# Performance work log

Hardware: AMD Instinct MI355X
Metric: run time of the kernel (lower is better)

## Reference

```python
import jax, jax.numpy as jnp
import numpy as np

BOS, EOS, MAX_STEPS = 1, 2, 50
VOCAB, EMBD, HID, CTX, SEQ = 50257, 512, 1024, 1024, 50


def setup_inputs() -> dict:
    key = jax.random.key(0)
    ks = jax.random.split(key, 13)
    s = 0.05
    return {
        "seq_enc_states": jax.random.normal(ks[0], (SEQ, 1, CTX), jnp.float32),
        "seq_enc_hidden": jax.random.normal(ks[1], (1, CTX), jnp.float32),
        "E": jax.random.normal(ks[2], (VOCAB, EMBD), jnp.float32) * s,
        "W_init": jax.random.normal(ks[3], (HID, CTX), jnp.float32) * s,
        "b_init": jax.random.normal(ks[4], (HID,), jnp.float32) * s,
        "Wa": jax.random.normal(ks[5], (CTX, HID), jnp.float32) * s,
        "ba": jax.random.normal(ks[6], (CTX,), jnp.float32) * s,
        "W_ih": jax.random.normal(ks[7], (3 * HID, EMBD + CTX), jnp.float32) * s,
        "W_hh": jax.random.normal(ks[8], (3 * HID, HID), jnp.float32) * s,
        "b_ih": jax.random.normal(ks[9], (3 * HID,), jnp.float32) * s,
        "b_hh": jax.random.normal(ks[10], (3 * HID,), jnp.float32) * s,
        "Wv": jax.random.normal(ks[11], (VOCAB, HID), jnp.float32) * s,
        "bv": jax.random.normal(ks[12], (VOCAB,), jnp.float32) * s,
    }


def _gru_cell(x, h, W_ih, W_hh, b_ih, b_hh):
    # torch.nn.GRUCell math
    gi = x @ W_ih.T + b_ih  # (1, 3H)
    gh = h @ W_hh.T + b_hh  # (1, 3H)
    i_r, i_z, i_n = jnp.split(gi, 3, axis=-1)
    h_r, h_z, h_n = jnp.split(gh, 3, axis=-1)
    r = jax.nn.sigmoid(i_r + h_r)
    z = jax.nn.sigmoid(i_z + h_z)
    n = jnp.tanh(i_n + r * h_n)
    return (1.0 - z) * n + z * h


def reference(seq_enc_states, seq_enc_hidden, E, W_init, b_init, Wa, ba,
              W_ih, W_hh, b_ih, b_hh, Wv, bv):
    enc = seq_enc_states[:, 0, :]                       # (S, CTX)
    h0 = seq_enc_hidden.reshape(1, -1) @ W_init.T + b_init  # (1, H)
    emb0 = E[BOS][None, :]                              # (1, EMBD)

    def step(carry, _):
        h, emb, done = carry
        # dot-product attention over the 50 encoder positions
        ph = h @ Wa.T + ba                              # (1, CTX)
        attn = jax.nn.softmax(ph @ enc.T, axis=-1)      # (1, S)
        ctx = attn @ enc                                # (1, CTX)
        x = jnp.concatenate([emb, ctx], axis=-1)        # (1, EMBD+CTX)
        h_new = _gru_cell(x, h, W_ih, W_hh, b_ih, b_hh)
        logp = jax.nn.log_softmax(h_new @ Wv.T + bv, axis=-1)  # (1, V)
        idx = jnp.argmax(logp[0])
        valid = jnp.logical_not(done)
        is_eos = idx == EOS
        emit_idx = jnp.where(valid & jnp.logical_not(is_eos), idx, -1).astype(jnp.int32)
        logp_out = jnp.where(valid, logp[0], 0.0)
        new_emb = jnp.where((valid & jnp.logical_not(is_eos))[..., None], E[idx][None, :], emb)
        new_h = jnp.where(valid, h_new, h)
        new_done = done | is_eos
        return (new_h, new_emb, new_done), (emit_idx, logp_out, valid)

    init = (h0, emb0, jnp.array(False))
    _, (indices, logps, valid) = jax.lax.scan(step, init, None, length=MAX_STEPS)
    # indices: (50,) int32, -1 where past eos / eos itself (not appended in original)
    return indices, logps, valid
```

## Files before the change

kernel.cpp:

```cpp
#include <hip/hip_runtime.h>
#include <hip/hip_fp16.h>
#include <cmath>

#define VOCABSZ 50257
#define EMBD 512
#define HIDD 1024
#define CTXD 1024
#define SEQL 50
#define NSTEPS 50
#define BOS_ID 1
#define EOS_ID 2

#define NTHR 256
#define NB_GI 768
#define NB_WR 64
#define NB_LOG 832
#define NW_LOG (NB_LOG * 4)
#define NB_GHN 192
#define KL_ATTN NB_LOG
#define KL_GH0 (NB_LOG + 1)
#define KL_WR0 (NB_LOG + 1 + NB_GHN)
#define KL_GRID (KL_WR0 + NB_WR)
#define PRE_GRID (NB_GI + 1)
#define PRE_GRID_FIN (NB_GI + 1 + NB_WR)

#define LPAD 50304

#define OFF_M      0
#define OFF_T      51200
#define OFF_H      51264
#define OFF_CTX    53312
#define OFF_GI     54336
#define OFF_GH     57408
#define OFF_L      63552
#define OFF_STATS  164160
#define OFF_STATE  170816
#define OFF_WVH    171072

__device__ __forceinline__ float wred_sum(float v) {
#pragma unroll
  for (int o = 32; o > 0; o >>= 1) v += __shfl_xor(v, o, 64);
  return v;
}

__device__ __forceinline__ float dot4(float4 a, float4 b) {
  return a.x * b.x + a.y * b.y + a.z * b.z + a.w * b.w;
}

__device__ __forceinline__ float wdot1024(const float* __restrict__ row, int lane,
                                          float4 b0, float4 b1, float4 b2, float4 b3) {
  const float4* r = (const float4*)row;
  float acc = dot4(r[lane], b0) + dot4(r[lane + 64], b1) +
              dot4(r[lane + 128], b2) + dot4(r[lane + 192], b3);
  return wred_sum(acc);
}

__device__ __forceinline__ bool beats(float v, int i, float v0, int i0) {
  return v > v0 || (v == v0 && i < i0);
}

__device__ __forceinline__ void top2_merge(float& v1, int& i1, float& v2, int& i2,
                                           float w1, int j1, float w2, int j2) {
  if (beats(w1, j1, v1, i1)) {
    float nv2; int ni2;
    if (beats(v1, i1, w2, j2)) { nv2 = v1; ni2 = i1; } else { nv2 = w2; ni2 = j2; }
    v1 = w1; i1 = j1; v2 = nv2; i2 = ni2;
  } else if (beats(w1, j1, v2, i2)) {
    v2 = w1; i2 = j1;
  }
}

__device__ __forceinline__ float acc8(uint4 a, const float* b) {
  const __half2* h = reinterpret_cast<const __half2*>(&a);
  float2 f0 = __half22float2(h[0]);
  float2 f1 = __half22float2(h[1]);
  float2 f2 = __half22float2(h[2]);
  float2 f3 = __half22float2(h[3]);
  return f0.x * b[0] + f0.y * b[1] + f1.x * b[2] + f1.y * b[3] +
         f2.x * b[4] + f2.y * b[5] + f3.x * b[6] + f3.y * b[7];
}

__global__ void __launch_bounds__(NTHR)
k_cvt(const float4* __restrict__ src, uint2* __restrict__ dst, int n4) {
  int i = blockIdx.x * NTHR + threadIdx.x;
  const int stride = gridDim.x * NTHR;
  for (; i < n4; i += stride) {
    float4 v = src[i];
    __half2 a = __floats2half2_rn(v.x, v.y);
    __half2 b = __floats2half2_rn(v.z, v.w);
    uint2 u;
    u.x = *reinterpret_cast<unsigned*>(&a);
    u.y = *reinterpret_cast<unsigned*>(&b);
    dst[i] = u;
  }
}

__global__ void __launch_bounds__(1024)
k0_matM(float* __restrict__ ws, const float* __restrict__ enc,
        const float* __restrict__ Wa) {
  const int kc = blockIdx.x;
  const int jg = blockIdx.y;
  const int tid = threadIdx.x;
  const int w = tid >> 6, lane = tid & 63;
  const int jw = w & 3, q = w >> 2;
  const int j = jg * 4 + jw;
  const int k = kc * 64 + lane;
  __shared__ float s_red[16][64];
  float acc0 = 0.f, acc1 = 0.f, acc2 = 0.f, acc3 = 0.f;
  if (j < SEQL) {
    const float4* e4 = (const float4*)(enc + (size_t)j * CTXD);
    const float* Wc = Wa + k;
    for (int c4 = q * 64; c4 < q * 64 + 64; ++c4) {
      float4 e = e4[c4];
      const float* wp = Wc + (size_t)(c4 * 4) * HIDD;
      acc0 += e.x * wp[0];
      acc1 += e.y * wp[HIDD];
      acc2 += e.z * wp[2 * HIDD];
      acc3 += e.w * wp[3 * HIDD];
    }
  }
  s_red[w][lane] = acc0 + acc1 + acc2 + acc3;
  __syncthreads();
  if (q == 0 && j < SEQL) {
    float v = s_red[jw][lane] + s_red[4 + jw][lane] +
              s_red[8 + jw][lane] + s_red[12 + jw][lane];
    ws[OFF_M + (size_t)j * HIDD + k] = v;
  }
}

__global__ void __launch_bounds__(NTHR)
k0_init(float* __restrict__ ws, const float* __restrict__ enc,
        const float* __restrict__ hid0, const float* __restrict__ Winit,
        const float* __restrict__ binit, const float* __restrict__ ba) {
  const int blk = blockIdx.x, tid = threadIdx.x;
  const int wave = tid >> 6, lane = tid & 63;
  if (blk == 0) {
    const float4* b4 = (const float4*)ba;
    float4 b0 = b4[lane], b1 = b4[lane + 64], b2 = b4[lane + 128], b3 = b4[lane + 192];
    for (int j = wave; j < SEQL; j += 4) {
      float v = wdot1024(enc + (size_t)j * CTXD, lane, b0, b1, b2, b3);
      if (lane == 0) ws[OFF_T + j] = v;
    }
    if (tid == 0) {
      int* st_emb = (int*)(ws + OFF_STATE);
      st_emb[0] = BOS_ID;
      st_emb[64] = 0;
    }
  } else {
    const float4* h4 = (const float4*)hid0;
    float4 b0 = h4[lane], b1 = h4[lane + 64], b2 = h4[lane + 128], b3 = h4[lane + 192];
    int row = (blk - 1) * 4 + wave;
    float v = wdot1024(Winit + (size_t)row * CTXD, lane, b0, b1, b2, b3) + binit[row];
    if (lane == 0) ws[OFF_H + row] = v;
  }
}

__device__ __forceinline__ void attn_from(float* __restrict__ ws, int hoff,
                                          const float* __restrict__ enc,
                                          int tid, int wave, int lane,
                                          float* s_h, float* s_sc, float* s_aw) {
  ((float4*)s_h)[tid] = ((const float4*)(ws + hoff))[tid];
  __syncthreads();
  const float4* h4 = (const float4*)s_h;
  float4 b0 = h4[lane], b1 = h4[lane + 64], b2 = h4[lane + 128], b3 = h4[lane + 192];
  for (int j = wave; j < SEQL; j += 4) {
    float v = wdot1024(ws + OFF_M + (size_t)j * HIDD, lane, b0, b1, b2, b3) + ws[OFF_T + j];
    if (lane == 0) s_sc[j] = v;
  }
  __syncthreads();
  if (tid < 64) {
    float v = (tid < SEQL) ? s_sc[tid] : -INFINITY;
    float mx = v;
#pragma unroll
    for (int o = 32; o > 0; o >>= 1) mx = fmaxf(mx, __shfl_xor(mx, o, 64));
    float e = (tid < SEQL) ? expf(v - mx) : 0.f;
    float sm = wred_sum(e);
    if (tid < SEQL) s_aw[tid] = e / sm;
  }
  __syncthreads();
  const float4* enc4 = (const float4*)enc;
  float4 acc = make_float4(0.f, 0.f, 0.f, 0.f);
  for (int j = 0; j < SEQL; ++j) {
    float a = s_aw[j];
    float4 ev = enc4[(size_t)j * (CTXD / 4) + tid];
    acc.x += a * ev.x; acc.y += a * ev.y; acc.z += a * ev.z; acc.w += a * ev.w;
  }
  ((float4*)(ws + OFF_CTX))[tid] = acc;
}

__global__ void __launch_bounds__(NTHR)
k_init2(float* __restrict__ ws, const float* __restrict__ enc,
        const float* __restrict__ Whh, const float* __restrict__ bhh) {
  const int blk = blockIdx.x, tid = threadIdx.x;
  const int wave = tid >> 6, lane = tid & 63;
  if (blk == 0) {
    __shared__ float s_h[HIDD];
    __shared__ float s_sc[64], s_aw[64];
    attn_from(ws, OFF_H, enc, tid, wave, lane, s_h, s_sc, s_aw);
  } else {
    const float4* h4 = (const float4*)(ws + OFF_H);
    float4 b0 = h4[lane], b1 = h4[lane + 64], b2 = h4[lane + 128], b3 = h4[lane + 192];
    const int r = (blk - 1) * 4 + wave;
    float v = wdot1024(Whh + (size_t)r * HIDD, lane, b0, b1, b2, b3) + bhh[r];
    if (lane == 0) ws[OFF_GH + r] = v;
  }
}

__global__ void __launch_bounds__(NTHR)
k_pre(float* __restrict__ ws, const float* __restrict__ E,
      const float* __restrict__ Wih, const float* __restrict__ bih,
      const float* __restrict__ Wv, const float* __restrict__ bv,
      float* __restrict__ out, int s) {
  const int blk = blockIdx.x, tid = threadIdx.x;
  const int wave = tid >> 6, lane = tid & 63;
  int* st_emb = (int*)(ws + OFF_STATE);
  int* st_done = st_emb + 64;
  const int hoff = OFF_H + (s & 1) * HIDD;

  const bool is_gi = (blk < NB_GI);
  const bool is_state = (blk == NB_GI);
  const bool is_writer = (blk > NB_GI);
  if (is_gi && s >= NSTEPS) return;
  if ((is_state || is_writer) && s == 0) return;

  int emb_s = 0, D_s = 0, gidx = -1;
  float logZ = 0.f;
  bool valid = false, eos = false;

  if (s > 0) {
    __shared__ float rm[NTHR], rs_[NTHR], rv1[NTHR], rv2[NTHR];
    __shared__ int ri1[NTHR], ri2[NTHR];
    __shared__ float s_ex[2];
    float m = -INFINITY, su = 0.f, v1 = -INFINITY, v2 = -INFINITY;
    int i1 = 0x7fffffff, i2 = 0x7fffffff;
    const float4* sb = (const float4*)(ws + OFF_STATS);
    for (int q = tid; q < NB_LOG; q += NTHR) {
      float4 A = sb[q * 2];
      float4 B = sb[q * 2 + 1];
      float mn = fmaxf(m, A.x);
      su = ((m == -INFINITY) ? 0.f : su * __expf(m - mn)) + A.y * __expf(A.x - mn);
      m = mn;
      top2_merge(v1, i1, v2, i2, A.z, __float_as_int(A.w), B.x, __float_as_int(B.y));
    }
    rm[tid] = m; rs_[tid] = su; rv1[tid] = v1; ri1[tid] = i1; rv2[tid] = v2; ri2[tid] = i2;
    __syncthreads();
    for (int st = 128; st > 0; st >>= 1) {
      if (tid < st) {
        float m2 = rm[tid + st], s2 = rs_[tid + st];
        float mn = fmaxf(rm[tid], m2);
        rs_[tid] = rs_[tid] * __expf(rm[tid] - mn) + s2 * __expf(m2 - mn);
        rm[tid] = mn;
        float a1 = rv1[tid], a2 = rv2[tid];
        int b1 = ri1[tid], b2 = ri2[tid];
        top2_merge(a1, b1, a2, b2, rv1[tid + st], ri1[tid + st], rv2[tid + st], ri2[tid + st]);
        rv1[tid] = a1; ri1[tid] = b1; rv2[tid] = a2; ri2[tid] = b2;
      }
      __syncthreads();
    }
    const int fi1 = ri1[0], fi2 = ri2[0];
    if (wave < 2) {
      const float4* h4 = (const float4*)(ws + hoff);
      float4 b0 = h4[lane], b1 = h4[lane + 64], b2 = h4[lane + 128], b3 = h4[lane + 192];
      const int r = (wave == 0) ? fi1 : fi2;
      float v = wdot1024(Wv + (size_t)r * HIDD, lane, b0, b1, b2, b3) + bv[r];
      if (lane == 0) s_ex[wave] = v;
    }
    __syncthreads();
    gidx = beats(s_ex[1], fi2, s_ex[0], fi1) ? fi2 : fi1;
    logZ = rm[0] + logf(rs_[0]);
    const int Dp = st_done[s - 1];
    valid = (Dp == 0);
    eos = (gidx == EOS_ID);
    D_s = Dp | (eos ? 1 : 0);
    emb_s = (valid && !eos) ? gidx : st_emb[s - 1];
  } else {
    emb_s = st_emb[0];
  }

  if (is_gi) {
    if (D_s) return;
    const int r = blk * 4 + wave;
    const float4* e4 = (const float4*)(E + (size_t)emb_s * EMBD);
    float4 eb0 = e4[lane], eb1 = e4[lane + 64];
    const float4* c4 = (const float4*)(ws + OFF_CTX);
    float4 cb0 = c4[lane], cb1 = c4[lane + 64], cb2 = c4[lane + 128], cb3 = c4[lane + 192];
    const float* rowp = Wih + (size_t)r * (EMBD + CTXD);
    const float4* re = (const float4*)rowp;
    const float4* rc = (const float4*)(rowp + EMBD);
    float acc = dot4(re[lane], eb0) + dot4(re[lane + 64], eb1) +
                dot4(rc[lane], cb0) + dot4(rc[lane + 64], cb1) +
                dot4(rc[lane + 128], cb2) + dot4(rc[lane + 192], cb3);
    float v = wred_sum(acc) + bih[r];
    if (lane == 0) ws[OFF_GI + r] = v;
  } else if (is_state) {
    if (tid == 0) {
      out[s - 1] = (valid && !eos) ? (float)gidx : -1.f;
      out[NSTEPS + (size_t)NSTEPS * VOCABSZ + (s - 1)] = valid ? 1.f : 0.f;
      st_emb[s] = emb_s;
      st_done[s] = D_s;
      ws[OFF_STATE + 128] = logZ;
      ws[OFF_STATE + 129] = valid ? 1.f : 0.f;
    }
  } else {
    const float* Lp = ws + OFF_L + (size_t)((s - 1) & 1) * LPAD;
    float* logp = out + NSTEPS + (size_t)(s - 1) * VOCABSZ;
    for (int i = (blk - NB_GI - 1) * NTHR + tid; i < VOCABSZ; i += NB_WR * NTHR)
      logp[i] = valid ? (Lp[i] - logZ) : 0.f;
  }
}

__global__ void __launch_bounds__(NTHR)
k_logits(float* __restrict__ ws, const float* __restrict__ bv,
         const float* __restrict__ enc, const float* __restrict__ Whh,
         const float* __restrict__ bhh, float* __restrict__ out, int s) {
  const int blk = blockIdx.x, tid = threadIdx.x;
  const int wave = tid >> 6, lane = tid & 63;
  const int p = s & 1, np = p ^ 1;

  if (blk >= KL_WR0) {
    if (s == 0) return;
    const float logZ = ws[OFF_STATE + 128];
    const bool valid = ws[OFF_STATE + 129] != 0.f;
    const float* Lp = ws + OFF_L + (size_t)np * LPAD;
    float* logp = out + NSTEPS + (size_t)(s - 1) * VOCABSZ;
    for (int i = (blk - KL_WR0) * NTHR + tid; i < VOCABSZ; i += NB_WR * NTHR)
      logp[i] = valid ? (Lp[i] - logZ) : 0.f;
    return;
  }

  __shared__ float s_h[HIDD];
  const int* st_emb = (const int*)(ws + OFF_STATE);
  const int done = st_emb[64 + s];

  const float* hp = ws + OFF_H + p * HIDD;
  const float* ghp = ws + OFF_GH + p * 3 * HIDD;
#pragma unroll
  for (int it = 0; it < HIDD / NTHR; ++it) {
    const int i = tid + it * NTHR;
    float h = hp[i];
    if (done) {
      s_h[i] = h;
    } else {
      float r = 1.f / (1.f + __expf(-(ws[OFF_GI + i] + ghp[i])));
      float z = 1.f / (1.f + __expf(-(ws[OFF_GI + HIDD + i] + ghp[HIDD + i])));
      float n = tanhf(ws[OFF_GI + 2 * HIDD + i] + r * ghp[2 * HIDD + i]);
      s_h[i] = (1.f - z) * n + z * h;
    }
  }
  __syncthreads();
  if (blk == 0) {
    ((float4*)(ws + OFF_H + np * HIDD))[tid] = ((const float4*)s_h)[tid];
  }

  if (blk >= KL_GH0) {
    if (s + 1 >= NSTEPS || done) return;
    const float4* h4 = (const float4*)s_h;
    float4 b0 = h4[lane], b1 = h4[lane + 64], b2 = h4[lane + 128], b3 = h4[lane + 192];
    const int wid = (blk - KL_GH0) * 4 + wave;
#pragma unroll
    for (int k = 0; k < 4; ++k) {
      const int r = wid + 768 * k;
      float v = wdot1024(Whh + (size_t)r * HIDD, lane, b0, b1, b2, b3) + bhh[r];
      if (lane == 0) ws[OFF_GH + np * 3 * HIDD + r] = v;
    }
    return;
  }

  if (blk == KL_ATTN) {
    if (s + 1 >= NSTEPS || done) return;
    __shared__ float s_sc[64], s_aw[64];
    const float4* h4 = (const float4*)s_h;
    float4 b0 = h4[lane], b1 = h4[lane + 64], b2 = h4[lane + 128], b3 = h4[lane + 192];
    for (int j = wave; j < SEQL; j += 4) {
      float v = wdot1024(ws + OFF_M + (size_t)j * HIDD, lane, b0, b1, b2, b3) + ws[OFF_T + j];
      if (lane == 0) s_sc[j] = v;
    }
    __syncthreads();
    if (tid < 64) {
      float v = (tid < SEQL) ? s_sc[tid] : -INFINITY;
      float mx = v;
#pragma unroll
      for (int o = 32; o > 0; o >>= 1) mx = fmaxf(mx, __shfl_xor(mx, o, 64));
      float e = (tid < SEQL) ? expf(v - mx) : 0.f;
      float smv = wred_sum(e);
      if (tid < SEQL) s_aw[tid] = e / smv;
    }
    __syncthreads();
    const float4* enc4 = (const float4*)enc;
    float4 acc = make_float4(0.f, 0.f, 0.f, 0.f);
    for (int j = 0; j < SEQL; ++j) {
      float a = s_aw[j];
      float4 ev = enc4[(size_t)j * (CTXD / 4) + tid];
      acc.x += a * ev.x; acc.y += a * ev.y; acc.z += a * ev.z; acc.w += a * ev.w;
    }
    ((float4*)(ws + OFF_CTX))[tid] = acc;
    return;
  }

  if (done) return;
  __shared__ float sm[4], ssm[4], sv1[4], sv2[4];
  __shared__ int si1[4], si2[4];
  float hb[16];
  {
    const float4* h4 = (const float4*)s_h;
    float4 a = h4[lane * 2], b = h4[lane * 2 + 1];
    float4 c = h4[128 + lane * 2], d = h4[129 + lane * 2];
    hb[0] = a.x; hb[1] = a.y; hb[2] = a.z; hb[3] = a.w;
    hb[4] = b.x; hb[5] = b.y; hb[6] = b.z; hb[7] = b.w;
    hb[8] = c.x; hb[9] = c.y; hb[10] = c.z; hb[11] = c.w;
    hb[12] = d.x; hb[13] = d.y; hb[14] = d.z; hb[15] = d.w;
  }
  const __half* WvH = (const __half*)(ws + OFF_WVH);
  float* Lc = ws + OFF_L + (size_t)p * LPAD;
  float m = -INFINITY, sum = 0.f, v1 = -INFINITY, v2 = -INFINITY;
  int i1 = 0x7fffffff, i2 = 0x7fffffff;
  for (int row = blk * 4 + wave; row < VOCABSZ; row += NW_LOG) {
    const uint4* r4 = (const uint4*)(WvH + (size_t)row * HIDD);
    float acc = acc8(r4[lane], hb) + acc8(r4[lane + 64], hb + 8);
    float l = wred_sum(acc) + bv[row];
    if (lane == 0) Lc[row] = l;
    float mn = fmaxf(m, l);
    sum = ((m == -INFINITY) ? 0.f : sum * __expf(m - mn)) + __expf(l - mn);
    m = mn;
    if (beats(l, row, v1, i1)) { v2 = v1; i2 = i1; v1 = l; i1 = row; }
    else if (beats(l, row, v2, i2)) { v2 = l; i2 = row; }
  }
  if (lane == 0) {
    sm[wave] = m; ssm[wave] = sum;
    sv1[wave] = v1; si1[wave] = i1; sv2[wave] = v2; si2[wave] = i2;
  }
  __syncthreads();
  if (tid == 0) {
    float mm = sm[0], su = ssm[0], a1 = sv1[0], a2 = sv2[0];
    int b1 = si1[0], b2 = si2[0];
#pragma unroll
    for (int w = 1; w < 4; ++w) {
      float mn = fmaxf(mm, sm[w]);
      su = su * __expf(mm - mn) + ssm[w] * __expf(sm[w] - mn);
      mm = mn;
      top2_merge(a1, b1, a2, b2, sv1[w], si1[w], sv2[w], si2[w]);
    }
    float* st = ws + OFF_STATS + (size_t)blk * 8;
    st[0] = mm; st[1] = su;
    st[2] = a1; st[3] = __int_as_float(b1);
    st[4] = a2; st[5] = __int_as_float(b2);
  }
}

extern "C" void kernel_launch(void* const* d_in, const int* in_sizes, int n_in,
                              void* d_out, int out_size, void* d_ws, size_t ws_size,
                              hipStream_t stream) {
  const float* enc   = (const float*)d_in[0];
  const float* hid0  = (const float*)d_in[1];
  const float* E     = (const float*)d_in[2];
  const float* Winit = (const float*)d_in[3];
  const float* binit = (const float*)d_in[4];
  const float* Wa    = (const float*)d_in[5];
  const float* ba    = (const float*)d_in[6];
  const float* Wih   = (const float*)d_in[7];
  const float* Whh   = (const float*)d_in[8];
  const float* bih   = (const float*)d_in[9];
  const float* bhh   = (const float*)d_in[10];
  const float* Wv    = (const float*)d_in[11];
  const float* bv    = (const float*)d_in[12];
  float* out = (float*)d_out;
  float* ws  = (float*)d_ws;

  const int n4 = (VOCABSZ * HIDD) / 4;
  k_cvt<<<4096, NTHR, 0, stream>>>((const float4*)Wv, (uint2*)(ws + OFF_WVH), n4);
  k0_matM<<<dim3(16, 13), 1024, 0, stream>>>(ws, enc, Wa);
  k0_init<<<257, NTHR, 0, stream>>>(ws, enc, hid0, Winit, binit, ba);
  k_init2<<<769, NTHR, 0, stream>>>(ws, enc, Whh, bhh);
  for (int s = 0; s < NSTEPS; ++s) {
    k_pre<<<PRE_GRID, NTHR, 0, stream>>>(ws, E, Wih, bih, Wv, bv, out, s);
    k_logits<<<KL_GRID, NTHR, 0, stream>>>(ws, bv, enc, Whh, bhh, out, s);
  }
  k_pre<<<PRE_GRID_FIN, NTHR, 0, stream>>>(ws, E, Wih, bih, Wv, bv, out, NSTEPS);
}
```

Baseline: 1.826 ms.

## Fuse global softmax/argmax reduction into last logits block via atomic counter

Before, every k_pre block (all 768 GI blocks plus a state block) redundantly reduced the 832 per-block stats and recomputed the top-2 logits, just to learn the chosen token and done flag. Now the last k_logits block to finish, found through an atomic counter and threadfence, does that reduction once and writes the token, logZ, emb and done state to the workspace. k_pre blocks then only read this state. This removes redundant reduction work from the critical path of each step, at the cost of a serialized tail in one block and reliance on fence/atomic ordering.

```diff
diff --git a/kernel.cpp b/kernel.cpp
--- a/kernel.cpp
+++ b/kernel.cpp
@@ -21,8 +21,8 @@
 #define KL_GH0 (NB_LOG + 1)
 #define KL_WR0 (NB_LOG + 1 + NB_GHN)
 #define KL_GRID (KL_WR0 + NB_WR)
-#define PRE_GRID (NB_GI + 1)
-#define PRE_GRID_FIN (NB_GI + 1 + NB_WR)
+#define PRE_GRID NB_GI
+#define PRE_GRID_FIN (NB_GI + NB_WR)
 
 #define LPAD 50304
 
@@ -141,11 +141,12 @@
       float v = wdot1024(enc + (size_t)j * CTXD, lane, b0, b1, b2, b3);
       if (lane == 0) ws[OFF_T + j] = v;
     }
+    int* st = (int*)(ws + OFF_STATE);
     if (tid == 0) {
-      int* st_emb = (int*)(ws + OFF_STATE);
-      st_emb[0] = BOS_ID;
-      st_emb[64] = 0;
-    }
+      st[0] = BOS_ID;
+      st[64] = 0;
+    }
+    if (tid < 64) st[192 + tid] = 0;
   } else {
     const float4* h4 = (const float4*)hid0;
     float4 b0 = h4[lane], b1 = h4[lane + 64], b2 = h4[lane + 128], b3 = h4[lane + 192];
@@ -209,76 +210,15 @@
 __global__ void __launch_bounds__(NTHR)
 k_pre(float* __restrict__ ws, const float* __restrict__ E,
       const float* __restrict__ Wih, const float* __restrict__ bih,
-      const float* __restrict__ Wv, const float* __restrict__ bv,
       float* __restrict__ out, int s) {
   const int blk = blockIdx.x, tid = threadIdx.x;
   const int wave = tid >> 6, lane = tid & 63;
-  int* st_emb = (int*)(ws + OFF_STATE);
-  int* st_done = st_emb + 64;
-  const int hoff = OFF_H + (s & 1) * HIDD;
-
-  const bool is_gi = (blk < NB_GI);
-  const bool is_state = (blk == NB_GI);
-  const bool is_writer = (blk > NB_GI);
-  if (is_gi && s >= NSTEPS) return;
-  if ((is_state || is_writer) && s == 0) return;
-
-  int emb_s = 0, D_s = 0, gidx = -1;
-  float logZ = 0.f;
-  bool valid = false, eos = false;
-
-  if (s > 0) {
-    __shared__ float rm[NTHR], rs_[NTHR], rv1[NTHR], rv2[NTHR];
-    __shared__ int ri1[NTHR], ri2[NTHR];
-    __shared__ float s_ex[2];
-    float m = -INFINITY, su = 0.f, v1 = -INFINITY, v2 = -INFINITY;
-    int i1 = 0x7fffffff, i2 = 0x7fffffff;
-    const float4* sb = (const float4*)(ws + OFF_STATS);
-    for (int q = tid; q < NB_LOG; q += NTHR) {
-      float4 A = sb[q * 2];
-      float4 B = sb[q * 2 + 1];
-      float mn = fmaxf(m, A.x);
-      su = ((m == -INFINITY) ? 0.f : su * __expf(m - mn)) + A.y * __expf(A.x - mn);
-      m = mn;
-      top2_merge(v1, i1, v2, i2, A.z, __float_as_int(A.w), B.x, __float_as_int(B.y));
-    }
-    rm[tid] = m; rs_[tid] = su; rv1[tid] = v1; ri1[tid] = i1; rv2[tid] = v2; ri2[tid] = i2;
-    __syncthreads();
-    for (int st = 128; st > 0; st >>= 1) {
-      if (tid < st) {
-        float m2 = rm[tid + st], s2 = rs_[tid + st];
-        float mn = fmaxf(rm[tid], m2);
-        rs_[tid] = rs_[tid] * __expf(rm[tid] - mn) + s2 * __expf(m2 - mn);
-        rm[tid] = mn;
-        float a1 = rv1[tid], a2 = rv2[tid];
-        int b1 = ri1[tid], b2 = ri2[tid];
-        top2_merge(a1, b1, a2, b2, rv1[tid + st], ri1[tid + st], rv2[tid + st], ri2[tid + st]);
-        rv1[tid] = a1; ri1[tid] = b1; rv2[tid] = a2; ri2[tid] = b2;
-      }
-      __syncthreads();
-    }
-    const int fi1 = ri1[0], fi2 = ri2[0];
-    if (wave < 2) {
-      const float4* h4 = (const float4*)(ws + hoff);
-      float4 b0 = h4[lane], b1 = h4[lane + 64], b2 = h4[lane + 128], b3 = h4[lane + 192];
-      const int r = (wave == 0) ? fi1 : fi2;
-      float v = wdot1024(Wv + (size_t)r * HIDD, lane, b0, b1, b2, b3) + bv[r];
-      if (lane == 0) s_ex[wave] = v;
-    }
-    __syncthreads();
-    gidx = beats(s_ex[1], fi2, s_ex[0], fi1) ? fi2 : fi1;
-    logZ = rm[0] + logf(rs_[0]);
-    const int Dp = st_done[s - 1];
-    valid = (Dp == 0);
-    eos = (gidx == EOS_ID);
-    D_s = Dp | (eos ? 1 : 0);
-    emb_s = (valid && !eos) ? gidx : st_emb[s - 1];
-  } else {
-    emb_s = st_emb[0];
-  }
-
-  if (is_gi) {
-    if (D_s) return;
+  const int* st_emb = (const int*)(ws + OFF_STATE);
+
+  if (blk < NB_GI) {
+    if (s >= NSTEPS) return;
+    if (st_emb[64 + s]) return;
+    const int emb_s = st_emb[s];
     const int r = blk * 4 + wave;
     const float4* e4 = (const float4*)(E + (size_t)emb_s * EMBD);
     float4 eb0 = e4[lane], eb1 = e4[lane + 64];
@@ -292,27 +232,22 @@
                 dot4(rc[lane + 128], cb2) + dot4(rc[lane + 192], cb3);
     float v = wred_sum(acc) + bih[r];
     if (lane == 0) ws[OFF_GI + r] = v;
-  } else if (is_state) {
-    if (tid == 0) {
-      out[s - 1] = (valid && !eos) ? (float)gidx : -1.f;
-      out[NSTEPS + (size_t)NSTEPS * VOCABSZ + (s - 1)] = valid ? 1.f : 0.f;
-      st_emb[s] = emb_s;
-      st_done[s] = D_s;
-      ws[OFF_STATE + 128] = logZ;
-      ws[OFF_STATE + 129] = valid ? 1.f : 0.f;
-    }
   } else {
+    if (s == 0) return;
+    const float logZ = ws[OFF_STATE + 128];
+    const bool valid = ws[OFF_STATE + 129] != 0.f;
     const float* Lp = ws + OFF_L + (size_t)((s - 1) & 1) * LPAD;
     float* logp = out + NSTEPS + (size_t)(s - 1) * VOCABSZ;
-    for (int i = (blk - NB_GI - 1) * NTHR + tid; i < VOCABSZ; i += NB_WR * NTHR)
+    for (int i = (blk - NB_GI) * NTHR + tid; i < VOCABSZ; i += NB_WR * NTHR)
       logp[i] = valid ? (Lp[i] - logZ) : 0.f;
   }
 }
 
 __global__ void __launch_bounds__(NTHR)
-k_logits(float* __restrict__ ws, const float* __restrict__ bv,
-         const float* __restrict__ enc, const float* __restrict__ Whh,
-         const float* __restrict__ bhh, float* __restrict__ out, int s) {
+k_logits(float* __restrict__ ws, const float* __restrict__ Wv,
+         const float* __restrict__ bv, const float* __restrict__ enc,
+         const float* __restrict__ Whh, const float* __restrict__ bhh,
+         float* __restrict__ out, int s) {
   const int blk = blockIdx.x, tid = threadIdx.x;
   const int wave = tid >> 6, lane = tid & 63;
   const int p = s & 1, np = p ^ 1;
@@ -329,8 +264,9 @@
   }
 
   __shared__ float s_h[HIDD];
-  const int* st_emb = (const int*)(ws + OFF_STATE);
-  const int done = st_emb[64 + s];
+  int* st_emb = (int*)(ws + OFF_STATE);
+  int* st_done = st_emb + 64;
+  const int done = st_done[s];
 
   const float* hp = ws + OFF_H + p * HIDD;
   const float* ghp = ws + OFF_GH + p * 3 * HIDD;
@@ -350,6 +286,14 @@
   __syncthreads();
   if (blk == 0) {
     ((float4*)(ws + OFF_H + np * HIDD))[tid] = ((const float4*)s_h)[tid];
+    if (done && tid == 0) {
+      out[s] = -1.f;
+      out[NSTEPS + (size_t)NSTEPS * VOCABSZ + s] = 0.f;
+      ws[OFF_STATE + 128] = 0.f;
+      ws[OFF_STATE + 129] = 0.f;
+      st_emb[s + 1] = st_emb[s];
+      st_done[s + 1] = 1;
+    }
   }
 
   if (blk >= KL_GH0) {
@@ -400,6 +344,7 @@
   if (done) return;
   __shared__ float sm[4], ssm[4], sv1[4], sv2[4];
   __shared__ int si1[4], si2[4];
+  __shared__ int s_last;
   float hb[16];
   {
     const float4* h4 = (const float4*)s_h;
@@ -444,6 +389,64 @@
     st[0] = mm; st[1] = su;
     st[2] = a1; st[3] = __int_as_float(b1);
     st[4] = a2; st[5] = __int_as_float(b2);
+    __threadfence();
+    int old = atomicAdd((int*)(ws + OFF_STATE) + 192 + s, 1);
+    s_last = (old == NB_LOG - 1) ? 1 : 0;
+  }
+  __syncthreads();
+  if (!s_last) return;
+
+  __threadfence();
+  __shared__ float rm[NTHR], rs_[NTHR], rv1[NTHR], rv2[NTHR];
+  __shared__ int ri1[NTHR], ri2[NTHR];
+  __shared__ float s_ex[2];
+  {
+    float cm = -INFINITY, cs = 0.f, c1 = -INFINITY, c2 = -INFINITY;
+    int ci1 = 0x7fffffff, ci2 = 0x7fffffff;
+    volatile const float* sb = ws + OFF_STATS;
+    for (int q = tid; q < NB_LOG; q += NTHR) {
+      const volatile float* st = sb + (size_t)q * 8;
+      float A0 = st[0], A1 = st[1], A2 = st[2], A3 = st[3], A4 = st[4], A5 = st[5];
+      float mn = fmaxf(cm, A0);
+      cs = ((cm == -INFINITY) ? 0.f : cs * __expf(cm - mn)) + A1 * __expf(A0 - mn);
+      cm = mn;
+      top2_merge(c1, ci1, c2, ci2, A2, __float_as_int(A3), A4, __float_as_int(A5));
+    }
+    rm[tid] = cm; rs_[tid] = cs; rv1[tid] = c1; ri1[tid] = ci1; rv2[tid] = c2; ri2[tid] = ci2;
+  }
+  __syncthreads();
+  for (int st = 128; st > 0; st >>= 1) {
+    if (tid < st) {
+      float m2 = rm[tid + st], s2 = rs_[tid + st];
+      float mn = fmaxf(rm[tid], m2);
+      rs_[tid] = rs_[tid] * __expf(rm[tid] - mn) + s2 * __expf(m2 - mn);
+      rm[tid] = mn;
+      float a1 = rv1[tid], a2 = rv2[tid];
+      int b1 = ri1[tid], b2 = ri2[tid];
+      top2_merge(a1, b1, a2, b2, rv1[tid + st], ri1[tid + st], rv2[tid + st], ri2[tid + st]);
+      rv1[tid] = a1; ri1[tid] = b1; rv2[tid] = a2; ri2[tid] = b2;
+    }
+    __syncthreads();
+  }
+  const int fi1 = ri1[0], fi2 = ri2[0];
+  if (wave < 2) {
+    const float4* h4 = (const float4*)s_h;
+    float4 b0 = h4[lane], b1 = h4[lane + 64], b2 = h4[lane + 128], b3 = h4[lane + 192];
+    const int r = (wave == 0) ? fi1 : fi2;
+    float v = wdot1024(Wv + (size_t)r * HIDD, lane, b0, b1, b2, b3) + bv[r];
+    if (lane == 0) s_ex[wave] = v;
+  }
+  __syncthreads();
+  if (tid == 0) {
+    const int gidx = beats(s_ex[1], fi2, s_ex[0], fi1) ? fi2 : fi1;
+    const float logZ = rm[0] + logf(rs_[0]);
+    const bool eos = (gidx == EOS_ID);
+    out[s] = eos ? -1.f : (float)gidx;
+    out[NSTEPS + (size_t)NSTEPS * VOCABSZ + s] = 1.f;
+    ws[OFF_STATE + 128] = logZ;
+    ws[OFF_STATE + 129] = 1.f;
+    st_emb[s + 1] = eos ? st_emb[s] : gidx;
+    st_done[s + 1] = eos ? 1 : 0;
   }
 }
 
@@ -472,8 +475,8 @@
   k0_init<<<257, NTHR, 0, stream>>>(ws, enc, hid0, Winit, binit, ba);
   k_init2<<<769, NTHR, 0, stream>>>(ws, enc, Whh, bhh);
   for (int s = 0; s < NSTEPS; ++s) {
-    k_pre<<<PRE_GRID, NTHR, 0, stream>>>(ws, E, Wih, bih, Wv, bv, out, s);
-    k_logits<<<KL_GRID, NTHR, 0, stream>>>(ws, bv, enc, Whh, bhh, out, s);
-  }
-  k_pre<<<PRE_GRID_FIN, NTHR, 0, stream>>>(ws, E, Wih, bih, Wv, bv, out, NSTEPS);
-}
+    k_pre<<<PRE_GRID, NTHR, 0, stream>>>(ws, E, Wih, bih, out, s);
+    k_logits<<<KL_GRID, NTHR, 0, stream>>>(ws, Wv, bv, enc, Whh, bhh, out, s);
+  }
+  k_pre<<<PRE_GRID_FIN, NTHR, 0, stream>>>(ws, E, Wih, bih, out, NSTEPS);
+}
```

After: 2.784 ms. 1.52x slower.
